# Kernel optimization log

Hardware: AMD Instinct MI355X
Metric: run time of the kernel (lower is better)

Reference implementation:

```python
import jax, jax.numpy as jnp
import numpy as np

N_ATOMS = 100000
N_BONDS = 200000
MAX_NB = 6
N_ATOM_FEATS = 39
N_BOND_FEATS = 11
HIDDEN = 128
DEPTH = 6


def setup_inputs() -> dict:
    key = jax.random.key(0)
    k = jax.random.split(key, 8)
    fatoms = jax.random.normal(k[0], (N_ATOMS, N_ATOM_FEATS), dtype=jnp.float32)
    fbonds = jax.random.normal(k[1], (N_BONDS, N_ATOM_FEATS + N_BOND_FEATS), dtype=jnp.float32)
    agraph = jax.random.randint(k[2], (N_ATOMS, MAX_NB), 0, N_BONDS, dtype=jnp.int32)
    bgraph = jax.random.randint(k[3], (N_BONDS, MAX_NB), 0, N_BONDS, dtype=jnp.int32)
    s_i = 1.0 / np.sqrt(N_ATOM_FEATS + N_BOND_FEATS)
    s_h = 1.0 / np.sqrt(HIDDEN)
    s_o = 1.0 / np.sqrt(N_ATOM_FEATS + HIDDEN)
    W_i = jax.random.uniform(k[4], (HIDDEN, N_ATOM_FEATS + N_BOND_FEATS), jnp.float32, -s_i, s_i)
    W_h = jax.random.uniform(k[5], (HIDDEN, HIDDEN), jnp.float32, -s_h, s_h)
    W_o = jax.random.uniform(k[6], (HIDDEN, N_ATOM_FEATS + HIDDEN), jnp.float32, -s_o, s_o)
    b_o = jax.random.uniform(k[7], (HIDDEN,), jnp.float32, -s_o, s_o)
    return {"fatoms": fatoms, "fbonds": fbonds, "agraph": agraph, "bgraph": bgraph,
            "W_i": W_i, "W_h": W_h, "W_o": W_o, "b_o": b_o}


def reference(fatoms, fbonds, agraph, bgraph, W_i, W_h, W_o, b_o):
    # Input message per directed bond: [n_bonds, hidden]
    binput = fbonds @ W_i.T
    message = jax.nn.relu(binput)
    # Message passing: gather neighbor bond messages, sum, linear, residual-add input, ReLU
    for _ in range(DEPTH - 1):
        nei = jnp.take(message, bgraph, axis=0).sum(axis=1)   # [n_bonds, hidden]
        message = jax.nn.relu(binput + nei @ W_h.T)
    # Aggregate incoming bond messages per atom
    a_nei = jnp.take(message, agraph, axis=0).sum(axis=1)      # [n_atoms, hidden]
    atom_input = jnp.concatenate([fatoms, a_nei], axis=1)      # dropout is identity at eval
    atom_h = jax.nn.relu(atom_input @ W_o.T + b_o)
    return atom_h
```

## Files before the change

### kernel.cpp

```cpp
#include <hip/hip_runtime.h>

#define N_ATOMS   100000
#define N_BONDS   200000
#define MAX_NB    6
#define AF        39
#define BFEAT     50
#define H         128
#define DEPTH     6
#define KS_I      2
#define KS_IH     6
#define KS_O      6
#define FBW       64
#define FAW       64

typedef unsigned short ushort_t;
typedef unsigned int   uint_t;

typedef __attribute__((ext_vector_type(8))) _Float16 f16x8;
typedef __attribute__((ext_vector_type(4))) float    f32x4;

__device__ inline uint_t pkh(float lo, float hi) {
    uint_t r;
    asm("v_cvt_pkrtz_f16_f32 %0, %1, %2" : "=v"(r) : "v"(lo), "v"(hi));
    return r;
}
__device__ inline ushort_t f2h(float f) {
    union { _Float16 h; ushort_t u; } v; v.h = (_Float16)f; return v.u;
}
__device__ inline uint_t pkadd(uint_t a, uint_t b) {
    uint_t r;
    asm("v_pk_add_f16 %0, %1, %2" : "=v"(r) : "v"(a), "v"(b));
    return r;
}
__device__ inline void addq(uint4& a, uint4 v) {
    a.x = pkadd(a.x, v.x); a.y = pkadd(a.y, v.y);
    a.z = pkadd(a.z, v.z); a.w = pkadd(a.w, v.w);
}

__global__ __launch_bounds__(256) void k_pack(const float* __restrict__ W_i,
                                              const float* __restrict__ W_h,
                                              const float* __restrict__ W_o,
                                              ushort_t* __restrict__ pWi,
                                              ushort_t* __restrict__ pWih,
                                              ushort_t* __restrict__ pWo) {
    int id = blockIdx.x * 256 + threadIdx.x;
    int mat;
    ushort_t* dst;
    if (id < 1024)      { mat = 0; dst = pWi; }
    else if (id < 4096) { mat = 1; dst = pWih; id -= 1024; }
    else                { mat = 2; dst = pWo;  id -= 4096; }
    const int lane = id & 63;
    const int nt   = (id >> 6) & 7;
    const int ks   = id >> 9;
    const int n  = nt * 16 + (lane & 15);
    const int k0 = ks * 32 + (lane >> 4) * 8;
    float v[8];
#pragma unroll
    for (int j = 0; j < 8; ++j) {
        const int k = k0 + j;
        float x = 0.f;
        if (mat == 0) {
            if (k < BFEAT) x = W_i[n * BFEAT + k];
        } else if (mat == 1) {
            if (k < BFEAT)     x = W_i[n * BFEAT + k];
            else if (k >= FBW) x = W_h[n * H + (k - FBW)];
        } else {
            if (k < H)           x = W_o[(size_t)n * (AF + H) + AF + k];
            else if (k < H + AF) x = W_o[(size_t)n * (AF + H) + (k - H)];
        }
        v[j] = x;
    }
    uint4 u;
    u.x = pkh(v[0], v[1]); u.y = pkh(v[2], v[3]);
    u.z = pkh(v[4], v[5]); u.w = pkh(v[6], v[7]);
    ((uint4*)dst)[id] = u;
}

__global__ __launch_bounds__(256) void k_fab(const float* __restrict__ fatoms,
                                             ushort_t* __restrict__ fab) {
    const int t = threadIdx.x;
    const int a0 = blockIdx.x * 64;
    const int row = t >> 2;
    const int c0 = (t & 3) * 16;
    const int a = a0 + row;
    if (a >= N_ATOMS) return;
    float v[16];
#pragma unroll
    for (int j = 0; j < 16; ++j) {
        const int c = c0 + j;
        v[j] = (c < AF) ? fatoms[(size_t)a * AF + c] : 0.f;
    }
    uint4 u0, u1;
    u0.x = pkh(v[0],  v[1]);  u0.y = pkh(v[2],  v[3]);
    u0.z = pkh(v[4],  v[5]);  u0.w = pkh(v[6],  v[7]);
    u1.x = pkh(v[8],  v[9]);  u1.y = pkh(v[10], v[11]);
    u1.z = pkh(v[12], v[13]); u1.w = pkh(v[14], v[15]);
    *(uint4*)(fab + (size_t)a * FAW + c0)     = u0;
    *(uint4*)(fab + (size_t)a * FAW + c0 + 8) = u1;
}

__global__ __launch_bounds__(256) void k_binput(const float* __restrict__ fbonds,
                                                const ushort_t* __restrict__ pWi,
                                                ushort_t* __restrict__ fbb,
                                                ushort_t* __restrict__ msg0) {
    __shared__ __align__(16) ushort_t sAC[64][136];
    const int t = threadIdx.x;
    const int b0 = blockIdx.x * 64;

    for (int i = t; i < 64 * 25; i += 256) {
        const int row = i / 25, j = i % 25;
        const float2 v = *(const float2*)(fbonds + (size_t)(b0 + row) * BFEAT + j * 2);
        *(uint_t*)&sAC[row][j * 2] = pkh(v.x, v.y);
    }
    for (int i = t; i < 64 * 7; i += 256) {
        const int row = i / 7, c = BFEAT + (i % 7) * 2;
        *(uint_t*)&sAC[row][c] = 0u;
    }
    __syncthreads();

    for (int i = t; i < 64 * 8; i += 256) {
        const int row = i >> 3, c0 = (i & 7) * 8;
        *(uint4*)(fbb + (size_t)(b0 + row) * FBW + c0) = *(const uint4*)&sAC[row][c0];
    }

    const int w    = t >> 6;
    const int lane = t & 63;
    const int col  = lane & 15;
    const int kg   = lane >> 4;
    const int m    = 16 * w + col;

    f32x4 acc[8];
#pragma unroll
    for (int nt = 0; nt < 8; ++nt) acc[nt] = (f32x4){0.f, 0.f, 0.f, 0.f};
    f16x8 af[KS_I];
#pragma unroll
    for (int ks = 0; ks < KS_I; ++ks)
        af[ks] = *(const f16x8*)&sAC[m][ks * 32 + kg * 8];
#pragma unroll
    for (int ks = 0; ks < KS_I; ++ks) {
#pragma unroll
        for (int nt = 0; nt < 8; ++nt) {
            const f16x8 b = *(const f16x8*)(pWi + (((size_t)(ks * 8 + nt) * 64 + lane) * 8));
            acc[nt] = __builtin_amdgcn_mfma_f32_16x16x32_f16(af[ks], b, acc[nt], 0, 0, 0);
        }
    }
    __syncthreads();

    const int row0 = kg * 4;
#pragma unroll
    for (int nt = 0; nt < 8; ++nt)
#pragma unroll
        for (int r = 0; r < 4; ++r)
            sAC[16 * w + row0 + r][nt * 16 + col] = f2h(fmaxf(acc[nt][r], 0.f));
    __syncthreads();

    for (int i = t; i < 64 * 16; i += 256) {
        const int row = i >> 4, c0 = (i & 15) * 8;
        *(uint4*)(msg0 + (size_t)(b0 + row) * H + c0) = *(const uint4*)&sAC[row][c0];
    }
}

__global__ __launch_bounds__(256) void k_mp(const ushort_t* __restrict__ msg_in,
                                            const int* __restrict__ bgraph,
                                            const ushort_t* __restrict__ pWih,
                                            const ushort_t* __restrict__ fbb,
                                            ushort_t* __restrict__ msg_out) {
    __shared__ __align__(16) ushort_t sAC[64][136];
    __shared__ int sIdx[64][MAX_NB];
    const int t = threadIdx.x;
    const int b0 = blockIdx.x * 64;

    for (int i = t; i < 64 * MAX_NB; i += 256)
        sIdx[i / MAX_NB][i % MAX_NB] = bgraph[(size_t)b0 * MAX_NB + i];
    __syncthreads();

    {
        const int bi = t >> 4;
        const int c0 = (t & 15) * 8;
#pragma unroll
        for (int p = 0; p < 4; p += 2) {
            const int iA = p * 16 + bi;
            const int iB = iA + 16;
            uint4 vA[MAX_NB], vB[MAX_NB];
#pragma unroll
            for (int j = 0; j < MAX_NB; ++j)
                vA[j] = *(const uint4*)(msg_in + (size_t)sIdx[iA][j] * H + c0);
#pragma unroll
            for (int j = 0; j < MAX_NB; ++j)
                vB[j] = *(const uint4*)(msg_in + (size_t)sIdx[iB][j] * H + c0);
            uint4 ua = vA[0], ub = vB[0];
#pragma unroll
            for (int j = 1; j < MAX_NB; ++j) addq(ua, vA[j]);
#pragma unroll
            for (int j = 1; j < MAX_NB; ++j) addq(ub, vB[j]);
            *(uint4*)&sAC[iA][c0] = ua;
            *(uint4*)&sAC[iB][c0] = ub;
        }
    }

    const int w    = t >> 6;
    const int lane = t & 63;
    const int col  = lane & 15;
    const int kg   = lane >> 4;
    const int m    = 16 * w + col;

    f16x8 af[KS_IH];
    af[0] = *(const f16x8*)(fbb + (size_t)(b0 + m) * FBW + kg * 8);
    af[1] = *(const f16x8*)(fbb + (size_t)(b0 + m) * FBW + 32 + kg * 8);
    __syncthreads();
#pragma unroll
    for (int ks = 2; ks < KS_IH; ++ks)
        af[ks] = *(const f16x8*)&sAC[m][(ks - 2) * 32 + kg * 8];

    f32x4 acc[8];
#pragma unroll
    for (int nt = 0; nt < 8; ++nt) acc[nt] = (f32x4){0.f, 0.f, 0.f, 0.f};
#pragma unroll
    for (int ks = 0; ks < KS_IH; ++ks) {
#pragma unroll
        for (int nt = 0; nt < 8; ++nt) {
            const f16x8 b = *(const f16x8*)(pWih + (((size_t)(ks * 8 + nt) * 64 + lane) * 8));
            acc[nt] = __builtin_amdgcn_mfma_f32_16x16x32_f16(af[ks], b, acc[nt], 0, 0, 0);
        }
    }
    const int row0 = kg * 4;
#pragma unroll
    for (int nt = 0; nt < 8; ++nt)
#pragma unroll
        for (int r = 0; r < 4; ++r)
            sAC[16 * w + row0 + r][nt * 16 + col] = f2h(fmaxf(acc[nt][r], 0.f));
    __syncthreads();

    for (int i = t; i < 64 * 16; i += 256) {
        const int row = i >> 4, c0 = (i & 15) * 8;
        *(uint4*)(msg_out + (size_t)(b0 + row) * H + c0) = *(const uint4*)&sAC[row][c0];
    }
}

__global__ __launch_bounds__(256) void k_out(const ushort_t* __restrict__ msg,
                                             const int* __restrict__ agraph,
                                             const ushort_t* __restrict__ fab,
                                             const ushort_t* __restrict__ pWo,
                                             const float* __restrict__ b_o,
                                             float* __restrict__ out) {
    __shared__ __align__(16) unsigned char smem[64 * 136 * 2];
    ushort_t (*sA)[136] = (ushort_t(*)[136])smem;
    float    (*sCh)[68] = (float(*)[68])smem;
    __shared__ int sIdx[64][MAX_NB];
    const int t = threadIdx.x;
    const int a0 = blockIdx.x * 64;

    for (int i = t; i < 64 * MAX_NB; i += 256) {
        const int a = a0 + i / MAX_NB;
        sIdx[i / MAX_NB][i % MAX_NB] = (a < N_ATOMS) ? agraph[(size_t)a * MAX_NB + (i % MAX_NB)] : 0;
    }
    __syncthreads();

    {
        const int bi = t >> 4;
        const int c0 = (t & 15) * 8;
#pragma unroll
        for (int p = 0; p < 4; p += 2) {
            const int iA = p * 16 + bi;
            const int iB = iA + 16;
            uint4 vA[MAX_NB], vB[MAX_NB];
#pragma unroll
            for (int j = 0; j < MAX_NB; ++j)
                vA[j] = *(const uint4*)(msg + (size_t)sIdx[iA][j] * H + c0);
#pragma unroll
            for (int j = 0; j < MAX_NB; ++j)
                vB[j] = *(const uint4*)(msg + (size_t)sIdx[iB][j] * H + c0);
            uint4 ua = vA[0], ub = vB[0];
#pragma unroll
            for (int j = 1; j < MAX_NB; ++j) addq(ua, vA[j]);
#pragma unroll
            for (int j = 1; j < MAX_NB; ++j) addq(ub, vB[j]);
            *(uint4*)&sA[iA][c0] = ua;
            *(uint4*)&sA[iB][c0] = ub;
        }
    }

    const int w    = t >> 6;
    const int lane = t & 63;
    const int col  = lane & 15;
    const int kg   = lane >> 4;
    const int m    = 16 * w + col;
    const int am   = a0 + m;
    const size_t amc = (size_t)((am < N_ATOMS) ? am : 0);

    f16x8 af[KS_O];
    af[4] = *(const f16x8*)(fab + amc * FAW + kg * 8);
    af[5] = *(const f16x8*)(fab + amc * FAW + 32 + kg * 8);
    __syncthreads();
#pragma unroll
    for (int ks = 0; ks < 4; ++ks)
        af[ks] = *(const f16x8*)&sA[m][ks * 32 + kg * 8];

    f32x4 acc[8];
#pragma unroll
    for (int nt = 0; nt < 8; ++nt) acc[nt] = (f32x4){0.f, 0.f, 0.f, 0.f};
#pragma unroll
    for (int ks = 0; ks < KS_O; ++ks) {
#pragma unroll
        for (int nt = 0; nt < 8; ++nt) {
            const f16x8 b = *(const f16x8*)(pWo + (((size_t)(ks * 8 + nt) * 64 + lane) * 8));
            acc[nt] = __builtin_amdgcn_mfma_f32_16x16x32_f16(af[ks], b, acc[nt], 0, 0, 0);
        }
    }
    __syncthreads();

    const int row0 = kg * 4;
    const float4* bo4 = (const float4*)b_o;
#pragma unroll
    for (int half = 0; half < 2; ++half) {
#pragma unroll
        for (int nt = 0; nt < 4; ++nt)
#pragma unroll
            for (int r = 0; r < 4; ++r)
                sCh[16 * w + row0 + r][nt * 16 + col] = acc[half * 4 + nt][r];
        __syncthreads();
#pragma unroll
        for (int p = 0; p < 4; ++p) {
            const int i = t + p * 256;
            const int row = i >> 4, c0 = (i & 15) * 4;
            const int a = a0 + row;
            if (a < N_ATOMS) {
                float4 cv = *(const float4*)&sCh[row][c0];
                const float4 bv = bo4[(half * 64 + c0) >> 2];
                cv.x = fmaxf(cv.x + bv.x, 0.f); cv.y = fmaxf(cv.y + bv.y, 0.f);
                cv.z = fmaxf(cv.z + bv.z, 0.f); cv.w = fmaxf(cv.w + bv.w, 0.f);
                *(float4*)(out + (size_t)a * H + half * 64 + c0) = cv;
            }
        }
        if (half == 0) __syncthreads();
    }
}

extern "C" void kernel_launch(void* const* d_in, const int* in_sizes, int n_in,
                              void* d_out, int out_size, void* d_ws, size_t ws_size,
                              hipStream_t stream) {
    const float* fatoms = (const float*)d_in[0];
    const float* fbonds = (const float*)d_in[1];
    const int*   agraph = (const int*)d_in[2];
    const int*   bgraph = (const int*)d_in[3];
    const float* W_i    = (const float*)d_in[4];
    const float* W_h    = (const float*)d_in[5];
    const float* W_o    = (const float*)d_in[6];
    const float* b_o    = (const float*)d_in[7];
    float* out = (float*)d_out;

    const size_t MSG_BYTES = (size_t)N_BONDS * H * sizeof(ushort_t);
    const size_t FBB_BYTES = (size_t)N_BONDS * FBW * sizeof(ushort_t);
    const size_t FAB_BYTES = (size_t)N_ATOMS * FAW * sizeof(ushort_t);
    char* ws = (char*)d_ws;
    ushort_t* m0   = (ushort_t*)(ws);
    ushort_t* m1   = (ushort_t*)(ws + MSG_BYTES);
    ushort_t* fbb  = (ushort_t*)(ws + 2 * MSG_BYTES);
    ushort_t* fab  = (ushort_t*)(ws + 2 * MSG_BYTES + FBB_BYTES);
    char*     wb   = ws + 2 * MSG_BYTES + FBB_BYTES + FAB_BYTES;
    ushort_t* pWi  = (ushort_t*)(wb);
    ushort_t* pWih = (ushort_t*)(wb + 16 * 1024);
    ushort_t* pWo  = (ushort_t*)(wb + 64 * 1024);

    k_pack<<<28, 256, 0, stream>>>(W_i, W_h, W_o, pWi, pWih, pWo);
    k_fab<<<(N_ATOMS + 63) / 64, 256, 0, stream>>>(fatoms, fab);
    k_binput<<<N_BONDS / 64, 256, 0, stream>>>(fbonds, pWi, fbb, m0);

    ushort_t* cur = m0;
    ushort_t* nxt = m1;
    for (int d = 0; d < DEPTH - 1; ++d) {
        k_mp<<<N_BONDS / 64, 256, 0, stream>>>(cur, bgraph, pWih, fbb, nxt);
        ushort_t* tmp = cur; cur = nxt; nxt = tmp;
    }

    k_out<<<(N_ATOMS + 63) / 64, 256, 0, stream>>>(cur, agraph, fab, pWo, b_o, out);
}
```

Measured before the change: 461.8 us.

## Split MFMA N-tiles into halves and store results directly from registers

The message-passing and output kernels now compute the 128-wide output in two halves of four N-tiles each, which halves live accumulator registers. They write the ReLU results straight from MFMA registers to global memory instead of staging them through shared memory. The neighbor gather also processes one row group at a time instead of two, trading memory-level parallelism for fewer VGPRs. The aim is higher occupancy and fewer barriers. The cost is re-reading A fragments from LDS per half, and narrow scattered 2-byte/4-byte global stores replacing coalesced 16-byte stores.

```diff
diff --git a/kernel.cpp b/kernel.cpp
--- a/kernel.cpp
+++ b/kernel.cpp
@@ -165,7 +165,7 @@
                                             const ushort_t* __restrict__ pWih,
                                             const ushort_t* __restrict__ fbb,
                                             ushort_t* __restrict__ msg_out) {
-    __shared__ __align__(16) ushort_t sAC[64][136];
+    __shared__ __align__(16) ushort_t sA[64][136];
     __shared__ int sIdx[64][MAX_NB];
     const int t = threadIdx.x;
     const int b0 = blockIdx.x * 64;
@@ -178,23 +178,16 @@
         const int bi = t >> 4;
         const int c0 = (t & 15) * 8;
 #pragma unroll
-        for (int p = 0; p < 4; p += 2) {
+        for (int p = 0; p < 4; ++p) {
             const int iA = p * 16 + bi;
-            const int iB = iA + 16;
-            uint4 vA[MAX_NB], vB[MAX_NB];
+            uint4 v[MAX_NB];
 #pragma unroll
             for (int j = 0; j < MAX_NB; ++j)
-                vA[j] = *(const uint4*)(msg_in + (size_t)sIdx[iA][j] * H + c0);
-#pragma unroll
-            for (int j = 0; j < MAX_NB; ++j)
-                vB[j] = *(const uint4*)(msg_in + (size_t)sIdx[iB][j] * H + c0);
-            uint4 ua = vA[0], ub = vB[0];
-#pragma unroll
-            for (int j = 1; j < MAX_NB; ++j) addq(ua, vA[j]);
-#pragma unroll
-            for (int j = 1; j < MAX_NB; ++j) addq(ub, vB[j]);
-            *(uint4*)&sAC[iA][c0] = ua;
-            *(uint4*)&sAC[iB][c0] = ub;
+                v[j] = *(const uint4*)(msg_in + (size_t)sIdx[iA][j] * H + c0);
+            uint4 ua = v[0];
+#pragma unroll
+            for (int j = 1; j < MAX_NB; ++j) addq(ua, v[j]);
+            *(uint4*)&sA[iA][c0] = ua;
         }
     }
 
@@ -204,36 +197,35 @@
     const int kg   = lane >> 4;
     const int m    = 16 * w + col;
 
-    f16x8 af[KS_IH];
-    af[0] = *(const f16x8*)(fbb + (size_t)(b0 + m) * FBW + kg * 8);
-    af[1] = *(const f16x8*)(fbb + (size_t)(b0 + m) * FBW + 32 + kg * 8);
-    __syncthreads();
-#pragma unroll
-    for (int ks = 2; ks < KS_IH; ++ks)
-        af[ks] = *(const f16x8*)&sAC[m][(ks - 2) * 32 + kg * 8];
-
-    f32x4 acc[8];
-#pragma unroll
-    for (int nt = 0; nt < 8; ++nt) acc[nt] = (f32x4){0.f, 0.f, 0.f, 0.f};
-#pragma unroll
-    for (int ks = 0; ks < KS_IH; ++ks) {
-#pragma unroll
-        for (int nt = 0; nt < 8; ++nt) {
-            const f16x8 b = *(const f16x8*)(pWih + (((size_t)(ks * 8 + nt) * 64 + lane) * 8));
-            acc[nt] = __builtin_amdgcn_mfma_f32_16x16x32_f16(af[ks], b, acc[nt], 0, 0, 0);
-        }
-    }
-    const int row0 = kg * 4;
-#pragma unroll
-    for (int nt = 0; nt < 8; ++nt)
-#pragma unroll
-        for (int r = 0; r < 4; ++r)
-            sAC[16 * w + row0 + r][nt * 16 + col] = f2h(fmaxf(acc[nt][r], 0.f));
-    __syncthreads();
-
-    for (int i = t; i < 64 * 16; i += 256) {
-        const int row = i >> 4, c0 = (i & 15) * 8;
-        *(uint4*)(msg_out + (size_t)(b0 + row) * H + c0) = *(const uint4*)&sAC[row][c0];
+    const f16x8 af0 = *(const f16x8*)(fbb + (size_t)(b0 + m) * FBW + kg * 8);
+    const f16x8 af1 = *(const f16x8*)(fbb + (size_t)(b0 + m) * FBW + 32 + kg * 8);
+    __syncthreads();
+
+    const int rowb = b0 + 16 * w + kg * 4;
+#pragma unroll
+    for (int half = 0; half < 2; ++half) {
+        f32x4 acc[4];
+#pragma unroll
+        for (int nt = 0; nt < 4; ++nt) acc[nt] = (f32x4){0.f, 0.f, 0.f, 0.f};
+#pragma unroll
+        for (int ks = 0; ks < KS_IH; ++ks) {
+            f16x8 a;
+            if (ks == 0)      a = af0;
+            else if (ks == 1) a = af1;
+            else              a = *(const f16x8*)&sA[m][(ks - 2) * 32 + kg * 8];
+#pragma unroll
+            for (int nt = 0; nt < 4; ++nt) {
+                const f16x8 b = *(const f16x8*)(pWih +
+                    (((size_t)(ks * 8 + half * 4 + nt) * 64 + lane) * 8));
+                acc[nt] = __builtin_amdgcn_mfma_f32_16x16x32_f16(a, b, acc[nt], 0, 0, 0);
+            }
+        }
+#pragma unroll
+        for (int nt = 0; nt < 4; ++nt)
+#pragma unroll
+            for (int r = 0; r < 4; ++r)
+                msg_out[(size_t)(rowb + r) * H + (half * 4 + nt) * 16 + col] =
+                    f2h(fmaxf(acc[nt][r], 0.f));
     }
 }
 
@@ -243,9 +235,7 @@
                                              const ushort_t* __restrict__ pWo,
                                              const float* __restrict__ b_o,
                                              float* __restrict__ out) {
-    __shared__ __align__(16) unsigned char smem[64 * 136 * 2];
-    ushort_t (*sA)[136] = (ushort_t(*)[136])smem;
-    float    (*sCh)[68] = (float(*)[68])smem;
+    __shared__ __align__(16) ushort_t sA[64][136];
     __shared__ int sIdx[64][MAX_NB];
     const int t = threadIdx.x;
     const int a0 = blockIdx.x * 64;
@@ -260,23 +250,16 @@
         const int bi = t >> 4;
         const int c0 = (t & 15) * 8;
 #pragma unroll
-        for (int p = 0; p < 4; p += 2) {
+        for (int p = 0; p < 4; ++p) {
             const int iA = p * 16 + bi;
-            const int iB = iA + 16;
-            uint4 vA[MAX_NB], vB[MAX_NB];
+            uint4 v[MAX_NB];
 #pragma unroll
             for (int j = 0; j < MAX_NB; ++j)
-                vA[j] = *(const uint4*)(msg + (size_t)sIdx[iA][j] * H + c0);
-#pragma unroll
-            for (int j = 0; j < MAX_NB; ++j)
-                vB[j] = *(const uint4*)(msg + (size_t)sIdx[iB][j] * H + c0);
-            uint4 ua = vA[0], ub = vB[0];
-#pragma unroll
-            for (int j = 1; j < MAX_NB; ++j) addq(ua, vA[j]);
-#pragma unroll
-            for (int j = 1; j < MAX_NB; ++j) addq(ub, vB[j]);
+                v[j] = *(const uint4*)(msg + (size_t)sIdx[iA][j] * H + c0);
+            uint4 ua = v[0];
+#pragma unroll
+            for (int j = 1; j < MAX_NB; ++j) addq(ua, v[j]);
             *(uint4*)&sA[iA][c0] = ua;
-            *(uint4*)&sA[iB][c0] = ub;
         }
     }
 
@@ -288,51 +271,41 @@
     const int am   = a0 + m;
     const size_t amc = (size_t)((am < N_ATOMS) ? am : 0);
 
-    f16x8 af[KS_O];
-    af[4] = *(const f16x8*)(fab + amc * FAW + kg * 8);
-    af[5] = *(const f16x8*)(fab + amc * FAW + 32 + kg * 8);
-    __syncthreads();
-#pragma unroll
-    for (int ks = 0; ks < 4; ++ks)
-        af[ks] = *(const f16x8*)&sA[m][ks * 32 + kg * 8];
-
-    f32x4 acc[8];
-#pragma unroll
-    for (int nt = 0; nt < 8; ++nt) acc[nt] = (f32x4){0.f, 0.f, 0.f, 0.f};
-#pragma unroll
-    for (int ks = 0; ks < KS_O; ++ks) {
-#pragma unroll
-        for (int nt = 0; nt < 8; ++nt) {
-            const f16x8 b = *(const f16x8*)(pWo + (((size_t)(ks * 8 + nt) * 64 + lane) * 8));
-            acc[nt] = __builtin_amdgcn_mfma_f32_16x16x32_f16(af[ks], b, acc[nt], 0, 0, 0);
-        }
-    }
-    __syncthreads();
-
-    const int row0 = kg * 4;
-    const float4* bo4 = (const float4*)b_o;
+    const f16x8 af4 = *(const f16x8*)(fab + amc * FAW + kg * 8);
+    const f16x8 af5 = *(const f16x8*)(fab + amc * FAW + 32 + kg * 8);
+    __syncthreads();
+
+    const int rowb = a0 + 16 * w + kg * 4;
 #pragma unroll
     for (int half = 0; half < 2; ++half) {
+        float bias[4];
+#pragma unroll
+        for (int nt = 0; nt < 4; ++nt) bias[nt] = b_o[(half * 4 + nt) * 16 + col];
+        f32x4 acc[4];
+#pragma unroll
+        for (int nt = 0; nt < 4; ++nt) acc[nt] = (f32x4){0.f, 0.f, 0.f, 0.f};
+#pragma unroll
+        for (int ks = 0; ks < KS_O; ++ks) {
+            f16x8 a;
+            if (ks < 4)       a = *(const f16x8*)&sA[m][ks * 32 + kg * 8];
+            else if (ks == 4) a = af4;
+            else              a = af5;
+#pragma unroll
+            for (int nt = 0; nt < 4; ++nt) {
+                const f16x8 b = *(const f16x8*)(pWo +
+                    (((size_t)(ks * 8 + half * 4 + nt) * 64 + lane) * 8));
+                acc[nt] = __builtin_amdgcn_mfma_f32_16x16x32_f16(a, b, acc[nt], 0, 0, 0);
+            }
+        }
 #pragma unroll
         for (int nt = 0; nt < 4; ++nt)
 #pragma unroll
-            for (int r = 0; r < 4; ++r)
-                sCh[16 * w + row0 + r][nt * 16 + col] = acc[half * 4 + nt][r];
-        __syncthreads();
-#pragma unroll
-        for (int p = 0; p < 4; ++p) {
-            const int i = t + p * 256;
-            const int row = i >> 4, c0 = (i & 15) * 4;
-            const int a = a0 + row;
-            if (a < N_ATOMS) {
-                float4 cv = *(const float4*)&sCh[row][c0];
-                const float4 bv = bo4[(half * 64 + c0) >> 2];
-                cv.x = fmaxf(cv.x + bv.x, 0.f); cv.y = fmaxf(cv.y + bv.y, 0.f);
-                cv.z = fmaxf(cv.z + bv.z, 0.f); cv.w = fmaxf(cv.w + bv.w, 0.f);
-                *(float4*)(out + (size_t)a * H + half * 64 + c0) = cv;
+            for (int r = 0; r < 4; ++r) {
+                const int arow = rowb + r;
+                if (arow < N_ATOMS)
+                    out[(size_t)arow * H + (half * 4 + nt) * 16 + col] =
+                        fmaxf(acc[nt][r] + bias[nt], 0.f);
             }
-        }
-        if (half == 0) __syncthreads();
     }
 }
 
```

Measured after the change: 469.8 us. No clear change (+1.7%).
